# Optimization experiments

Measured on AMD Instinct MI355X. Metric: run time of the kernel, lower is better.

The kernel has to match this reference:

```python
import jax, jax.numpy as jnp
import numpy as np

N_NODES = 100000
N_EDGES = 1600000
IN_DIM = 128
HID = 64
OUT = 64


def setup_inputs() -> dict:
    key = jax.random.key(0)
    ks = jax.random.split(key, 8)
    feats = jax.random.normal(ks[0], (N_NODES, IN_DIM), dtype=jnp.float32)
    src = jax.random.randint(ks[1], (N_EDGES,), 0, N_NODES)
    dst = jax.random.randint(ks[2], (N_EDGES,), 0, N_NODES)
    W1 = jax.random.normal(ks[3], (IN_DIM, HID), dtype=jnp.float32) * (1.0 / np.sqrt(IN_DIM))
    b1 = jnp.zeros((HID,), jnp.float32)
    W2 = jax.random.normal(ks[4], (HID, HID), dtype=jnp.float32) * (1.0 / np.sqrt(HID))
    b2 = jnp.zeros((HID,), jnp.float32)
    Wout = jax.random.normal(ks[5], (2 * HID, OUT), dtype=jnp.float32) * (1.0 / np.sqrt(2 * HID))
    bout = jnp.zeros((OUT,), jnp.float32)
    return {"feats": feats, "src": src, "dst": dst, "W1": W1, "b1": b1,
            "W2": W2, "b2": b2, "Wout": Wout, "bout": bout}


def reference(feats, src, dst, W1, b1, W2, b2, Wout, bout):
    N = feats.shape[0]
    ones = jnp.ones(src.shape[0], dtype=feats.dtype)
    # DGL GraphConv norm='both': symmetric degree normalization, degrees clamped to >= 1
    deg_out = jnp.maximum(jax.ops.segment_sum(ones, src, num_segments=N), 1.0)
    deg_in = jnp.maximum(jax.ops.segment_sum(ones, dst, num_segments=N), 1.0)
    norm_s = deg_out ** -0.5  # [N]
    norm_d = deg_in ** -0.5   # [N]

    def gconv(x, W, b):
        h = (x * norm_s[:, None]) @ W                      # transform (order-equivalent)
        agg = jax.ops.segment_sum(h[src], dst, num_segments=N)  # sparse neighbor sum
        return jax.nn.relu(agg * norm_d[:, None] + b)

    h1 = gconv(feats, W1, b1)   # [N, HID]
    h2 = gconv(h1, W2, b2)      # [N, HID]
    jumped = jnp.concatenate([h1, h2], axis=-1)  # JK 'cat' -> [N, 2*HID]
    # Concate module: unnormalized copy_u/sum aggregation
    agged = jax.ops.segment_sum(jumped[src], dst, num_segments=N)
    return agged @ Wout + bout
```

## Files before the change

kernel.cpp:

```cpp
#include <hip/hip_runtime.h>

static inline int divup(long a, long b){ return (int)((a + b - 1) / b); }

typedef float f32x4 __attribute__((ext_vector_type(4)));

#define CAP    64
#define BSHIFT 9
#define BNODES 512
#define CAP_E  12288
#define PBLK   256


__global__ void k_zero32(unsigned* __restrict__ p, long n){
  long i = (long)blockIdx.x * blockDim.x + threadIdx.x;
  long st = (long)gridDim.x * blockDim.x;
  for (; i < n; i += st) p[i] = 0u;
}

__global__ __launch_bounds__(256) void k_part2(const int* __restrict__ src,
    const int* __restrict__ dst, int E, int per,
    int* __restrict__ curD, int* __restrict__ curS,
    unsigned* __restrict__ partD, int* __restrict__ partS)
{
  __shared__ int hD[256], hS[256];
  const int t = threadIdx.x;
  const int b0 = blockIdx.x * per, b1 = min(E, b0 + per);
  hD[t] = 0; hS[t] = 0;
  __syncthreads();
  for (int i = b0 + t; i < b1; i += 256){
    atomicAdd(&hD[dst[i] >> BSHIFT], 1);
    atomicAdd(&hS[src[i] >> BSHIFT], 1);
  }
  __syncthreads();
  { int c = hD[t]; hD[t] = c ? atomicAdd(&curD[t], c) : 0;
    c = hS[t];     hS[t] = c ? atomicAdd(&curS[t], c) : 0; }
  __syncthreads();
  for (int i = b0 + t; i < b1; i += 256){
    int s = src[i], d = dst[i];
    int bD = d >> BSHIFT;
    int p = atomicAdd(&hD[bD], 1);
    if (p < CAP_E)
      partD[(long)bD * CAP_E + p] = ((unsigned)(d & (BNODES - 1)) << 17) | (unsigned)s;
    int bS = s >> BSHIFT;
    int q = atomicAdd(&hS[bS], 1);
    if (q < CAP_E)
      partS[(long)bS * CAP_E + q] = s;
  }
}

__global__ __launch_bounds__(256) void k_csr_degs(const int* __restrict__ curD,
    const int* __restrict__ curS, unsigned* __restrict__ partD,
    const int* __restrict__ partS, int* __restrict__ rowptr,
    int* __restrict__ degD, int* __restrict__ degS, int N)
{
  __shared__ unsigned ed[CAP_E];
  __shared__ int cnt[BNODES], scn[BNODES], tmp[256];
  const int B = blockIdx.x, t = threadIdx.x;
  const long base = (long)B * CAP_E;
  int m = curD[B]; if (m > CAP_E) m = CAP_E;
  for (int i = t; i < BNODES; i += 256) cnt[i] = 0;
  __syncthreads();
  for (int i = t; i < m; i += 256){
    unsigned p = partD[base + i];
    ed[i] = p;
    atomicAdd(&cnt[p >> 17], 1);
  }
  __syncthreads();
  int a0 = cnt[2 * t], a1 = cnt[2 * t + 1];
  int s = a0 + a1;
  tmp[t] = s;
  __syncthreads();
  for (int off = 1; off < 256; off <<= 1){
    int v = (t >= off) ? tmp[t - off] : 0;
    __syncthreads();
    tmp[t] += v;
    __syncthreads();
  }
  int excl = tmp[t] - s;
  scn[2 * t]     = excl;
  scn[2 * t + 1] = excl + a0;
  __syncthreads();
  const int nodeBase = B << BSHIFT;
  for (int i = t; i < BNODES; i += 256){
    int node = nodeBase + i;
    if (node < N){ rowptr[node] = (int)base + scn[i]; degD[node] = cnt[i]; }
  }
  __syncthreads();
  int* csr = (int*)partD;
  for (int i = t; i < m; i += 256){
    unsigned p = ed[i];
    int slot = atomicAdd(&scn[p >> 17], 1);
    csr[base + slot] = (int)(p & 0x1FFFFu);
  }
  int mS = curS[B]; if (mS > CAP_E) mS = CAP_E;
  __syncthreads();
  for (int i = t; i < BNODES; i += 256) cnt[i] = 0;
  __syncthreads();
  for (int i = t; i < mS; i += 256)
    atomicAdd(&cnt[partS[base + i] & (BNODES - 1)], 1);
  __syncthreads();
  for (int i = t; i < BNODES; i += 256){
    int node = nodeBase + i;
    if (node < N) degS[node] = cnt[i];
  }
}

template<int MODE>
__global__ __launch_bounds__(256) void k_agg(const float* __restrict__ h,
    const int* __restrict__ rowptr, const int* __restrict__ degD,
    const int* __restrict__ csr, const float* __restrict__ bias,
    float* __restrict__ out, int N)
{
  int node = blockIdx.x * 4 + (threadIdx.x >> 6);
  if (node >= N) return;
  int lane = threadIdx.x & 63;
  int eg = lane >> 4;
  int c4 = (lane & 15) << 2;
  int beg = rowptr[node];
  int deg = degD[node];
  int end = beg + deg;

  float ax = 0.f, ay = 0.f, az = 0.f, aw = 0.f;
  float bx = 0.f, by = 0.f, bz = 0.f, bw = 0.f;
  int p = beg + eg;
  for (; p + 12 < end; p += 16){
    int s0 = __builtin_nontemporal_load(csr + p);
    int s1 = __builtin_nontemporal_load(csr + p + 4);
    int s2 = __builtin_nontemporal_load(csr + p + 8);
    int s3 = __builtin_nontemporal_load(csr + p + 12);
    float4 v0 = *(const float4*)&h[(long)s0 * 64 + c4];
    float4 v1 = *(const float4*)&h[(long)s1 * 64 + c4];
    float4 v2 = *(const float4*)&h[(long)s2 * 64 + c4];
    float4 v3 = *(const float4*)&h[(long)s3 * 64 + c4];
    ax += v0.x; ay += v0.y; az += v0.z; aw += v0.w;
    bx += v1.x; by += v1.y; bz += v1.z; bw += v1.w;
    ax += v2.x; ay += v2.y; az += v2.z; aw += v2.w;
    bx += v3.x; by += v3.y; bz += v3.z; bw += v3.w;
  }
  for (; p < end; p += 4){
    int s = __builtin_nontemporal_load(csr + p);
    float4 v = *(const float4*)&h[(long)s * 64 + c4];
    ax += v.x; ay += v.y; az += v.z; aw += v.w;
  }
  ax += bx; ay += by; az += bz; aw += bw;

  ax += __shfl_xor(ax, 16); ay += __shfl_xor(ay, 16);
  az += __shfl_xor(az, 16); aw += __shfl_xor(aw, 16);
  ax += __shfl_xor(ax, 32); ay += __shfl_xor(ay, 32);
  az += __shfl_xor(az, 32); aw += __shfl_xor(aw, 32);

  if (eg == 0){
    float4 bb = *(const float4*)&bias[c4];
    f32x4 r;
    if constexpr (MODE == 1){
      float nd = rsqrtf((float)(deg < 1 ? 1 : deg));
      r.x = fmaxf(fmaf(ax, nd, bb.x), 0.f);
      r.y = fmaxf(fmaf(ay, nd, bb.y), 0.f);
      r.z = fmaxf(fmaf(az, nd, bb.z), 0.f);
      r.w = fmaxf(fmaf(aw, nd, bb.w), 0.f);
    } else {
      r.x = ax + bb.x; r.y = ay + bb.y; r.z = az + bb.z; r.w = aw + bb.w;
    }
    __builtin_nontemporal_store(r, (f32x4*)&out[(long)node * 64 + c4]);
  }
}

template<int K0, int K1, bool SCALE>
__global__ __launch_bounds__(256) void k_gemm(
    const float* __restrict__ A0, const float* __restrict__ A1,
    const float* __restrict__ W, const int* __restrict__ degS,
    float* __restrict__ out, int N)
{
  constexpr int K = K0 + K1;
  __shared__ float sW[K * 64];
  const int tid  = threadIdx.x;
  const int brow = blockIdx.x * 64;
  const int tx = tid & 15, ty = tid >> 4;
  const int c0 = tx << 2;

  #pragma unroll
  for (int it = 0; it < K / 16; it++){
    int id = tid + it * 256;
    int k = id >> 4, c4 = (id & 15) << 2;
    *(float4*)&sW[k * 64 + c4] = *(const float4*)&W[k * 64 + c4];
  }

  const float* pa0[4];
  const float* pa1[4];
  float scale[4];
  #pragma unroll
  for (int i = 0; i < 4; i++){
    int row = brow + ty + 16 * i;
    int r = (row < N) ? row : 0;
    pa0[i] = A0 + (long)r * K0;
    if constexpr (K1 != 0) pa1[i] = A1 + (long)r * K1;
    if constexpr (SCALE){
      int dg = degS[r];
      scale[i] = rsqrtf((float)(dg < 1 ? 1 : dg));
    }
  }

  __syncthreads();

  float4 acc[4];
  #pragma unroll
  for (int i = 0; i < 4; i++) acc[i] = make_float4(0.f, 0.f, 0.f, 0.f);

  #pragma unroll 2
  for (int kk = 0; kk < K0 / 4; ++kk){
    float4 a[4];
    #pragma unroll
    for (int i = 0; i < 4; i++) a[i] = *(const float4*)&pa0[i][kk * 4];
    float4 w0 = *(const float4*)&sW[(4 * kk + 0) * 64 + c0];
    float4 w1 = *(const float4*)&sW[(4 * kk + 1) * 64 + c0];
    float4 w2 = *(const float4*)&sW[(4 * kk + 2) * 64 + c0];
    float4 w3 = *(const float4*)&sW[(4 * kk + 3) * 64 + c0];
    #pragma unroll
    for (int i = 0; i < 4; i++){
      acc[i].x += a[i].x * w0.x + a[i].y * w1.x + a[i].z * w2.x + a[i].w * w3.x;
      acc[i].y += a[i].x * w0.y + a[i].y * w1.y + a[i].z * w2.y + a[i].w * w3.y;
      acc[i].z += a[i].x * w0.z + a[i].y * w1.z + a[i].z * w2.z + a[i].w * w3.z;
      acc[i].w += a[i].x * w0.w + a[i].y * w1.w + a[i].z * w2.w + a[i].w * w3.w;
    }
  }
  if constexpr (K1 != 0){
    #pragma unroll 2
    for (int kk = 0; kk < K1 / 4; ++kk){
      float4 a[4];
      #pragma unroll
      for (int i = 0; i < 4; i++) a[i] = *(const float4*)&pa1[i][kk * 4];
      int kb = K0 + 4 * kk;
      float4 w0 = *(const float4*)&sW[(kb + 0) * 64 + c0];
      float4 w1 = *(const float4*)&sW[(kb + 1) * 64 + c0];
      float4 w2 = *(const float4*)&sW[(kb + 2) * 64 + c0];
      float4 w3 = *(const float4*)&sW[(kb + 3) * 64 + c0];
      #pragma unroll
      for (int i = 0; i < 4; i++){
        acc[i].x += a[i].x * w0.x + a[i].y * w1.x + a[i].z * w2.x + a[i].w * w3.x;
        acc[i].y += a[i].x * w0.y + a[i].y * w1.y + a[i].z * w2.y + a[i].w * w3.y;
        acc[i].z += a[i].x * w0.z + a[i].y * w1.z + a[i].z * w2.z + a[i].w * w3.z;
        acc[i].w += a[i].x * w0.w + a[i].y * w1.w + a[i].z * w2.w + a[i].w * w3.w;
      }
    }
  }

  #pragma unroll
  for (int i = 0; i < 4; i++){
    int row = brow + ty + 16 * i;
    if (row < N){
      f32x4 r;
      if constexpr (SCALE){
        r.x = acc[i].x * scale[i]; r.y = acc[i].y * scale[i];
        r.z = acc[i].z * scale[i]; r.w = acc[i].w * scale[i];
      } else {
        r.x = acc[i].x; r.y = acc[i].y; r.z = acc[i].z; r.w = acc[i].w;
      }
      *(f32x4*)&out[(long)row * 64 + c0] = r;
    }
  }
}


__global__ void k_prep(const int* __restrict__ src, const int* __restrict__ dst,
                       int* __restrict__ degS, int* __restrict__ degD,
                       int* __restrict__ padded, int E){
  int i = blockIdx.x * blockDim.x + threadIdx.x;
  if (i >= E) return;
  int s = src[i], d = dst[i];
  int slot = atomicAdd(&degD[d], 1);
  if (slot < CAP) padded[(long)d * CAP + slot] = s;
  atomicAdd(&degS[s], 1);
}

template<int MODE>
__global__ __launch_bounds__(256) void k_agg_pad(const float* __restrict__ h,
    const int* __restrict__ padded, const int* __restrict__ degD,
    const float* __restrict__ bias, float* __restrict__ out, int N)
{
  int node = blockIdx.x * 4 + (threadIdx.x >> 6);
  if (node >= N) return;
  int lane = threadIdx.x & 63;
  int deg = degD[node];
  int len = deg < CAP ? deg : CAP;
  const int* row = padded + (long)node * CAP;
  int sid = (lane < len) ? row[lane] : 0;
  float acc0 = 0.f, acc1 = 0.f;
  int t = 0;
  for (; t + 4 <= len; t += 4){
    int s0 = __shfl(sid, t),   s1 = __shfl(sid, t+1);
    int s2 = __shfl(sid, t+2), s3 = __shfl(sid, t+3);
    acc0 += h[(long)s0 * 64 + lane];
    acc1 += h[(long)s1 * 64 + lane];
    acc0 += h[(long)s2 * 64 + lane];
    acc1 += h[(long)s3 * 64 + lane];
  }
  for (; t < len; ++t){
    int s = __shfl(sid, t);
    acc0 += h[(long)s * 64 + lane];
  }
  float acc = acc0 + acc1;
  float r;
  if constexpr (MODE == 1){
    float nd = rsqrtf((float)(deg < 1 ? 1 : deg));
    r = fmaxf(fmaf(acc, nd, bias[lane]), 0.f);
  } else {
    r = acc + bias[lane];
  }
  out[(long)node * 64 + lane] = r;
}


extern "C" void kernel_launch(void* const* d_in, const int* in_sizes, int n_in,
                              void* d_out, int out_size, void* d_ws, size_t ws_size,
                              hipStream_t stream){
  const float* feats = (const float*)d_in[0];
  const int*   src   = (const int*)  d_in[1];
  const int*   dst   = (const int*)  d_in[2];
  const float* W1    = (const float*)d_in[3];
  const float* b1    = (const float*)d_in[4];
  const float* W2    = (const float*)d_in[5];
  const float* b2    = (const float*)d_in[6];
  const float* Wout  = (const float*)d_in[7];
  const float* bout  = (const float*)d_in[8];
  float* out = (float*)d_out;

  const int N = in_sizes[0] / 128;
  const int E = in_sizes[1];

  const int gemmGrid = divup(N, 64);
  const int aggGrid  = divup(N, 4);
  const int nb       = divup(N, BNODES);

  size_t needA = ((size_t)(3L * N) + 512
                + 2L * (size_t)nb * CAP_E
                + 192L * N) * 4;
  if (N <= 131072 && nb <= 256 && ws_size >= needA){
    int*      degS   = (int*)d_ws;
    int*      degD   = degS + N;
    int*      rowptr = degD + N;
    int*      curD   = rowptr + N;
    int*      curS   = curD + 256;
    unsigned* partD  = (unsigned*)(curS + 256);
    int*      partS  = (int*)(partD + (long)nb * CAP_E);
    float*    ht     = (float*)(partS + (long)nb * CAP_E);
    float*    h1     = ht + 64L * N;
    float*    h2     = h1 + 64L * N;
    int*      csr    = (int*)partD;

    k_zero32<<<1, 256, 0, stream>>>((unsigned*)curD, 512);
    k_part2<<<PBLK, 256, 0, stream>>>(src, dst, E, divup(E, PBLK), curD, curS, partD, partS);
    k_csr_degs<<<nb, 256, 0, stream>>>(curD, curS, partD, partS, rowptr, degD, degS, N);

    k_gemm<128, 0, true><<<gemmGrid, 256, 0, stream>>>(feats, nullptr, W1, degS, ht, N);
    k_agg<1><<<aggGrid, 256, 0, stream>>>(ht, rowptr, degD, csr, b1, h1, N);

    k_gemm<64, 0, true><<<gemmGrid, 256, 0, stream>>>(h1, nullptr, W2, degS, ht, N);
    k_agg<1><<<aggGrid, 256, 0, stream>>>(ht, rowptr, degD, csr, b2, h2, N);

    k_gemm<64, 64, false><<<gemmGrid, 256, 0, stream>>>(h1, h2, Wout, nullptr, ht, N);
    k_agg<0><<<aggGrid, 256, 0, stream>>>(ht, rowptr, degD, csr, bout, out, N);
    return;
  }

  int*   degS   = (int*)d_ws;
  int*   degD   = degS + N;
  int*   padded = degD + N;
  float* ht     = (float*)(padded + (long)CAP * N);
  float* h1     = ht + 64L * N;
  float* h2     = h1 + 64L * N;

  k_zero32<<<256, 256, 0, stream>>>((unsigned*)degS, 2L * N);
  k_prep<<<divup(E, 256), 256, 0, stream>>>(src, dst, degS, degD, padded, E);

  k_gemm<128, 0, true><<<gemmGrid, 256, 0, stream>>>(feats, nullptr, W1, degS, ht, N);
  k_agg_pad<1><<<aggGrid, 256, 0, stream>>>(ht, padded, degD, b1, h1, N);

  k_gemm<64, 0, true><<<gemmGrid, 256, 0, stream>>>(h1, nullptr, W2, degS, ht, N);
  k_agg_pad<1><<<aggGrid, 256, 0, stream>>>(ht, padded, degD, b2, h2, N);

  k_gemm<64, 64, false><<<gemmGrid, 256, 0, stream>>>(h1, h2, Wout, nullptr, ht, N);
  k_agg_pad<0><<<aggGrid, 256, 0, stream>>>(ht, padded, degD, bout, out, N);
}
```

Baseline: 355.4 us.

## Fuse per-node dense transforms into aggregation epilogues, dropping two GEMM launches

The second and third GEMMs (h1@W2 scaled by source norm, and [h1,h2]@Wout) now run inside the epilogue of the preceding aggregation kernel. Each wavefront redistributes its aggregated row across the 64 lanes and does a shuffle-broadcast matvec against weights read from global memory. This removes two kernel launches and the write and re-read of the h2 intermediate. In exchange, each lane does 64-128 serial shuffles plus FMAs with uncached, non-LDS weight reads, so the dense work runs as a per-node matvec instead of a tiled GEMM.

New measurement: 483.1 us. 1.36x slower.

```diff
diff --git a/kernel.cpp b/kernel.cpp
--- a/kernel.cpp
+++ b/kernel.cpp
@@ -105,22 +105,17 @@
   }
 }
 
-template<int MODE>
-__global__ __launch_bounds__(256) void k_agg(const float* __restrict__ h,
+__device__ __forceinline__ void gather_reduce(const float* __restrict__ h,
     const int* __restrict__ rowptr, const int* __restrict__ degD,
-    const int* __restrict__ csr, const float* __restrict__ bias,
-    float* __restrict__ out, int N)
-{
-  int node = blockIdx.x * 4 + (threadIdx.x >> 6);
-  if (node >= N) return;
-  int lane = threadIdx.x & 63;
+    const int* __restrict__ csr, int node, int lane,
+    float& ax, float& ay, float& az, float& aw, int& deg)
+{
   int eg = lane >> 4;
   int c4 = (lane & 15) << 2;
   int beg = rowptr[node];
-  int deg = degD[node];
+  deg = degD[node];
   int end = beg + deg;
-
-  float ax = 0.f, ay = 0.f, az = 0.f, aw = 0.f;
+  ax = 0.f; ay = 0.f; az = 0.f; aw = 0.f;
   float bx = 0.f, by = 0.f, bz = 0.f, bw = 0.f;
   int p = beg + eg;
   for (; p + 12 < end; p += 16){
@@ -143,24 +138,97 @@
     ax += v.x; ay += v.y; az += v.z; aw += v.w;
   }
   ax += bx; ay += by; az += bz; aw += bw;
-
   ax += __shfl_xor(ax, 16); ay += __shfl_xor(ay, 16);
   az += __shfl_xor(az, 16); aw += __shfl_xor(aw, 16);
   ax += __shfl_xor(ax, 32); ay += __shfl_xor(ay, 32);
   az += __shfl_xor(az, 32); aw += __shfl_xor(aw, 32);
-
-  if (eg == 0){
-    float4 bb = *(const float4*)&bias[c4];
+}
+
+__device__ __forceinline__ float row_to_lane(float ax, float ay, float az,
+                                             float aw, int lane)
+{
+  int q = lane >> 2, j = lane & 3;
+  float f0 = __shfl(ax, q), f1 = __shfl(ay, q);
+  float f2 = __shfl(az, q), f3 = __shfl(aw, q);
+  float r = (j == 0) ? f0 : (j == 1) ? f1 : (j == 2) ? f2 : f3;
+  return r;
+}
+
+__global__ __launch_bounds__(256) void k_agg1f(const float* __restrict__ ht,
+    const int* __restrict__ rowptr, const int* __restrict__ degD,
+    const int* __restrict__ csr, const float* __restrict__ b1,
+    const int* __restrict__ degS, const float* __restrict__ W2,
+    float* __restrict__ h1, float* __restrict__ ht2, int N)
+{
+  int node = blockIdx.x * 4 + (threadIdx.x >> 6);
+  if (node >= N) return;
+  int lane = threadIdx.x & 63;
+  float ax, ay, az, aw; int deg;
+  gather_reduce(ht, rowptr, degD, csr, node, lane, ax, ay, az, aw, deg);
+
+  float nd = rsqrtf((float)(deg < 1 ? 1 : deg));
+  float f  = row_to_lane(ax, ay, az, aw, lane);
+  float rv = fmaxf(fmaf(f, nd, b1[lane]), 0.f);
+  __builtin_nontemporal_store(rv, &h1[(long)node * 64 + lane]);
+
+  float acc = 0.f;
+  #pragma unroll 4
+  for (int k = 0; k < 64; ++k){
+    float hk = __shfl(rv, k);
+    acc = fmaf(hk, W2[k * 64 + lane], acc);
+  }
+  int dgs = degS[node];
+  float ns = rsqrtf((float)(dgs < 1 ? 1 : dgs));
+  ht2[(long)node * 64 + lane] = ns * acc;
+}
+
+__global__ __launch_bounds__(256) void k_agg2f(const float* __restrict__ ht2,
+    const int* __restrict__ rowptr, const int* __restrict__ degD,
+    const int* __restrict__ csr, const float* __restrict__ b2,
+    const float* __restrict__ h1, const float* __restrict__ Wout,
+    float* __restrict__ y, int N)
+{
+  int node = blockIdx.x * 4 + (threadIdx.x >> 6);
+  if (node >= N) return;
+  int lane = threadIdx.x & 63;
+  float h1v = h1[(long)node * 64 + lane];
+
+  float ax, ay, az, aw; int deg;
+  gather_reduce(ht2, rowptr, degD, csr, node, lane, ax, ay, az, aw, deg);
+
+  float nd = rsqrtf((float)(deg < 1 ? 1 : deg));
+  float f  = row_to_lane(ax, ay, az, aw, lane);
+  float rv = fmaxf(fmaf(f, nd, b2[lane]), 0.f);
+
+  float acc = 0.f;
+  #pragma unroll 4
+  for (int k = 0; k < 64; ++k){
+    float hk = __shfl(h1v, k);
+    acc = fmaf(hk, Wout[k * 64 + lane], acc);
+  }
+  #pragma unroll 4
+  for (int k = 0; k < 64; ++k){
+    float hk = __shfl(rv, k);
+    acc = fmaf(hk, Wout[(64 + k) * 64 + lane], acc);
+  }
+  y[(long)node * 64 + lane] = acc;
+}
+
+__global__ __launch_bounds__(256) void k_agg3(const float* __restrict__ y,
+    const int* __restrict__ rowptr, const int* __restrict__ degD,
+    const int* __restrict__ csr, const float* __restrict__ bout,
+    float* __restrict__ out, int N)
+{
+  int node = blockIdx.x * 4 + (threadIdx.x >> 6);
+  if (node >= N) return;
+  int lane = threadIdx.x & 63;
+  float ax, ay, az, aw; int deg;
+  gather_reduce(y, rowptr, degD, csr, node, lane, ax, ay, az, aw, deg);
+  if (lane < 16){
+    int c4 = lane << 2;
+    float4 bb = *(const float4*)&bout[c4];
     f32x4 r;
-    if constexpr (MODE == 1){
-      float nd = rsqrtf((float)(deg < 1 ? 1 : deg));
-      r.x = fmaxf(fmaf(ax, nd, bb.x), 0.f);
-      r.y = fmaxf(fmaf(ay, nd, bb.y), 0.f);
-      r.z = fmaxf(fmaf(az, nd, bb.z), 0.f);
-      r.w = fmaxf(fmaf(aw, nd, bb.w), 0.f);
-    } else {
-      r.x = ax + bb.x; r.y = ay + bb.y; r.z = az + bb.z; r.w = aw + bb.w;
-    }
+    r.x = ax + bb.x; r.y = ay + bb.y; r.z = az + bb.z; r.w = aw + bb.w;
     __builtin_nontemporal_store(r, (f32x4*)&out[(long)node * 64 + c4]);
   }
 }
@@ -344,21 +412,18 @@
     int*      partS  = (int*)(partD + (long)nb * CAP_E);
     float*    ht     = (float*)(partS + (long)nb * CAP_E);
     float*    h1     = ht + 64L * N;
-    float*    h2     = h1 + 64L * N;
+    float*    ht2    = h1 + 64L * N;
     int*      csr    = (int*)partD;
+    float*    y      = ht;
 
     k_zero32<<<1, 256, 0, stream>>>((unsigned*)curD, 512);
     k_part2<<<PBLK, 256, 0, stream>>>(src, dst, E, divup(E, PBLK), curD, curS, partD, partS);
     k_csr_degs<<<nb, 256, 0, stream>>>(curD, curS, partD, partS, rowptr, degD, degS, N);
 
     k_gemm<128, 0, true><<<gemmGrid, 256, 0, stream>>>(feats, nullptr, W1, degS, ht, N);
-    k_agg<1><<<aggGrid, 256, 0, stream>>>(ht, rowptr, degD, csr, b1, h1, N);
-
-    k_gemm<64, 0, true><<<gemmGrid, 256, 0, stream>>>(h1, nullptr, W2, degS, ht, N);
-    k_agg<1><<<aggGrid, 256, 0, stream>>>(ht, rowptr, degD, csr, b2, h2, N);
-
-    k_gemm<64, 64, false><<<gemmGrid, 256, 0, stream>>>(h1, h2, Wout, nullptr, ht, N);
-    k_agg<0><<<aggGrid, 256, 0, stream>>>(ht, rowptr, degD, csr, bout, out, N);
+    k_agg1f<<<aggGrid, 256, 0, stream>>>(ht, rowptr, degD, csr, b1, degS, W2, h1, ht2, N);
+    k_agg2f<<<aggGrid, 256, 0, stream>>>(ht2, rowptr, degD, csr, b2, h1, Wout, y, N);
+    k_agg3 <<<aggGrid, 256, 0, stream>>>(y, rowptr, degD, csr, bout, out, N);
     return;
   }
 
```

## Fuse edge partitioning and CSR build into one cooperative kernel with grid sync

Applied to the files above, without the earlier changes.

Merges the edge-partition kernel and the CSR/degree kernel into a single cooperative launch that uses a grid-wide sync between phases. The zeroing kernel becomes a hipMemsetAsync. Partitioning now runs with nb (196) blocks instead of 256, and it reuses the cnt/scn shared arrays for its histograms. The aim is to cut launch overhead and inter-kernel gaps. In exchange, the partition phase has slightly less parallelism and the kernel depends on cooperative launch with every block co-resident.

Measured after the change: 411.9 us. 15.9% more time.

```diff
diff --git a/kernel.cpp b/kernel.cpp
--- a/kernel.cpp
+++ b/kernel.cpp
@@ -1,4 +1,7 @@
 #include <hip/hip_runtime.h>
+#include <hip/hip_cooperative_groups.h>
+
+namespace cg = cooperative_groups;
 
 static inline int divup(long a, long b){ return (int)((a + b - 1) / b); }
 
@@ -8,7 +11,6 @@
 #define BSHIFT 9
 #define BNODES 512
 #define CAP_E  12288
-#define PBLK   256
 
 
 __global__ void k_zero32(unsigned* __restrict__ p, long n){
@@ -17,45 +19,44 @@
   for (; i < n; i += st) p[i] = 0u;
 }
 
-__global__ __launch_bounds__(256) void k_part2(const int* __restrict__ src,
-    const int* __restrict__ dst, int E, int per,
+__global__ __launch_bounds__(256) void k_prep_all(
+    const int* __restrict__ src, const int* __restrict__ dst,
+    int E, int N, int nb, int per,
     int* __restrict__ curD, int* __restrict__ curS,
-    unsigned* __restrict__ partD, int* __restrict__ partS)
-{
-  __shared__ int hD[256], hS[256];
-  const int t = threadIdx.x;
-  const int b0 = blockIdx.x * per, b1 = min(E, b0 + per);
-  hD[t] = 0; hS[t] = 0;
-  __syncthreads();
-  for (int i = b0 + t; i < b1; i += 256){
-    atomicAdd(&hD[dst[i] >> BSHIFT], 1);
-    atomicAdd(&hS[src[i] >> BSHIFT], 1);
-  }
-  __syncthreads();
-  { int c = hD[t]; hD[t] = c ? atomicAdd(&curD[t], c) : 0;
-    c = hS[t];     hS[t] = c ? atomicAdd(&curS[t], c) : 0; }
-  __syncthreads();
-  for (int i = b0 + t; i < b1; i += 256){
-    int s = src[i], d = dst[i];
-    int bD = d >> BSHIFT;
-    int p = atomicAdd(&hD[bD], 1);
-    if (p < CAP_E)
-      partD[(long)bD * CAP_E + p] = ((unsigned)(d & (BNODES - 1)) << 17) | (unsigned)s;
-    int bS = s >> BSHIFT;
-    int q = atomicAdd(&hS[bS], 1);
-    if (q < CAP_E)
-      partS[(long)bS * CAP_E + q] = s;
-  }
-}
-
-__global__ __launch_bounds__(256) void k_csr_degs(const int* __restrict__ curD,
-    const int* __restrict__ curS, unsigned* __restrict__ partD,
-    const int* __restrict__ partS, int* __restrict__ rowptr,
-    int* __restrict__ degD, int* __restrict__ degS, int N)
+    unsigned* __restrict__ partD, int* __restrict__ partS,
+    int* __restrict__ rowptr, int* __restrict__ degD, int* __restrict__ degS)
 {
   __shared__ unsigned ed[CAP_E];
   __shared__ int cnt[BNODES], scn[BNODES], tmp[256];
+  cg::grid_group grid = cg::this_grid();
   const int B = blockIdx.x, t = threadIdx.x;
+
+  {
+    const int b0 = B * per, b1 = min(E, b0 + per);
+    cnt[t] = 0; scn[t] = 0;
+    __syncthreads();
+    for (int i = b0 + t; i < b1; i += 256){
+      atomicAdd(&cnt[dst[i] >> BSHIFT], 1);
+      atomicAdd(&scn[src[i] >> BSHIFT], 1);
+    }
+    __syncthreads();
+    { int c = cnt[t]; cnt[t] = c ? atomicAdd(&curD[t], c) : 0;
+      c = scn[t];     scn[t] = c ? atomicAdd(&curS[t], c) : 0; }
+    __syncthreads();
+    for (int i = b0 + t; i < b1; i += 256){
+      int s = src[i], d = dst[i];
+      int bD = d >> BSHIFT;
+      int p = atomicAdd(&cnt[bD], 1);
+      if (p < CAP_E)
+        partD[(long)bD * CAP_E + p] = ((unsigned)(d & (BNODES - 1)) << 17) | (unsigned)s;
+      int bS = s >> BSHIFT;
+      int q = atomicAdd(&scn[bS], 1);
+      if (q < CAP_E)
+        partS[(long)bS * CAP_E + q] = s;
+    }
+  }
+  grid.sync();
+
   const long base = (long)B * CAP_E;
   int m = curD[B]; if (m > CAP_E) m = CAP_E;
   for (int i = t; i < BNODES; i += 256) cnt[i] = 0;
@@ -347,9 +348,22 @@
     float*    h2     = h1 + 64L * N;
     int*      csr    = (int*)partD;
 
-    k_zero32<<<1, 256, 0, stream>>>((unsigned*)curD, 512);
-    k_part2<<<PBLK, 256, 0, stream>>>(src, dst, E, divup(E, PBLK), curD, curS, partD, partS);
-    k_csr_degs<<<nb, 256, 0, stream>>>(curD, curS, partD, partS, rowptr, degD, degS, N);
+    hipMemsetAsync(curD, 0, 512 * sizeof(int), stream);
+
+    {
+      int E_ = E, N_ = N, nb_ = nb, per_ = divup(E, nb);
+      const int* src_ = src; const int* dst_ = dst;
+      int* curD_ = curD; int* curS_ = curS;
+      unsigned* partD_ = partD; int* partS_ = partS;
+      int* rowptr_ = rowptr; int* degD_ = degD; int* degS_ = degS;
+      void* args[] = { (void*)&src_, (void*)&dst_, (void*)&E_, (void*)&N_,
+                       (void*)&nb_, (void*)&per_,
+                       (void*)&curD_, (void*)&curS_,
+                       (void*)&partD_, (void*)&partS_,
+                       (void*)&rowptr_, (void*)&degD_, (void*)&degS_ };
+      hipLaunchCooperativeKernel((void*)k_prep_all, dim3(nb), dim3(256),
+                                 args, 0, stream);
+    }
 
     k_gemm<128, 0, true><<<gemmGrid, 256, 0, stream>>>(feats, nullptr, W1, degS, ht, N);
     k_agg<1><<<aggGrid, 256, 0, stream>>>(ht, rowptr, degD, csr, b1, h1, N);
```
